# Kernel optimization log

Hardware: AMD Instinct MI355X
Metric: run time of the kernel (lower is better)

## Reference

```python
import jax, jax.numpy as jnp
import numpy as np

B, S, C, H, F = 4, 2048, 256, 8, 512  # scenes, pillars/scene, embed, heads, ffn hidden
D = C // H


def setup_inputs() -> dict:
    key = jax.random.key(0)
    ks = jax.random.split(key, 6)
    n = lambda k, sh: jax.random.normal(k, sh, jnp.float32) * 0.02
    # batch index sorted, equal-size contiguous segments per scene
    bidx = (jnp.arange(B * S, dtype=jnp.int32) // S)[:, None]
    coords = jnp.concatenate([bidx, jnp.zeros((B * S, 3), jnp.int32)], axis=1)
    return dict(
        pillar_features=jax.random.normal(ks[0], (B * S, C), jnp.float32),
        voxel_coords=coords,
        w_qkv=n(ks[1], (3 * C, C)), b_qkv=jnp.zeros((3 * C,), jnp.float32),
        w_out=n(ks[2], (C, C)), b_out=jnp.zeros((C,), jnp.float32),
        ln1_g=jnp.ones((C,), jnp.float32), ln1_b=jnp.zeros((C,), jnp.float32),
        w1=n(ks[3], (F, C)), b1=jnp.zeros((F,), jnp.float32),
        w2=n(ks[4], (C, F)), b2=jnp.zeros((C,), jnp.float32),
        ln2_g=jnp.ones((C,), jnp.float32), ln2_b=jnp.zeros((C,), jnp.float32),
    )


def _ln(x, g, b):
    m = x.mean(-1, keepdims=True)
    v = x.var(-1, keepdims=True)  # biased var, matches torch LayerNorm
    return (x - m) / jnp.sqrt(v + 1e-5) * g + b


def reference(pillar_features, voxel_coords, w_qkv, b_qkv, w_out, b_out,
              ln1_g, ln1_b, w1, b1, w2, b2, ln2_g, ln2_b):
    # coords[:,0] is sorted with equal-size contiguous segments, so the
    # per-batch mask-gather in the original is exactly a reshape here.
    x = pillar_features.reshape(B, S, C)
    qkv = x @ w_qkv.T + b_qkv                      # [B,S,3C]
    q, k, v = jnp.split(qkv, 3, axis=-1)
    rs = lambda t: t.reshape(B, S, H, D).transpose(0, 2, 1, 3)  # [B,H,S,D]
    q, k, v = rs(q), rs(k), rs(v)
    scores = jnp.einsum('bhqd,bhkd->bhqk', q, k) / jnp.sqrt(jnp.float32(D))
    att = jax.nn.softmax(scores, axis=-1)
    o = jnp.einsum('bhqk,bhkd->bhqd', att, v).transpose(0, 2, 1, 3).reshape(B, S, C)
    o = o @ w_out.T + b_out
    x = _ln(x + o, ln1_g, ln1_b)
    f = jax.nn.gelu(x @ w1.T + b1, approximate=False) @ w2.T + b2
    x = _ln(x + f, ln2_g, ln2_b)
    return x.reshape(B * S, C)
```

## Files before the change

### kernel.cpp

```cpp
#include <hip/hip_runtime.h>
#include <math.h>

#define MROWS 8192
#define BATCH 4
#define SEQ   2048
#define CDIM  256
#define HEADS 8
#define DHEAD 32
#define FDIM  512
#define QKVN  768

typedef __attribute__((ext_vector_type(8))) short bf16x8;
typedef __attribute__((ext_vector_type(4))) float f32x4;

__device__ __forceinline__ unsigned pk_bf16(float a, float b) {
  unsigned r;
  asm("v_cvt_pk_bf16_f32 %0, %1, %2" : "=v"(r) : "v"(a), "v"(b));
  return r;
}
__device__ __forceinline__ float bf2f(short s) {
  unsigned u = ((unsigned)(unsigned short)s) << 16;
  return __builtin_bit_cast(float, u);
}
__device__ __forceinline__ float bflo(unsigned w) {
  return __builtin_bit_cast(float, w << 16);
}
__device__ __forceinline__ float bfhi(unsigned w) {
  return __builtin_bit_cast(float, w & 0xffff0000u);
}
__device__ __forceinline__ short f2bf(float f) {
  unsigned u = __builtin_bit_cast(unsigned, f);
  u = (u + 0x7FFFu + ((u >> 16) & 1u)) >> 16;
  return (short)u;
}
__device__ __forceinline__ float fexp2(float x) {
#if __has_builtin(__builtin_amdgcn_exp2f)
  return __builtin_amdgcn_exp2f(x);
#else
  return exp2f(x);
#endif
}
__device__ __forceinline__ void gl16(const void* g, void* l) {
  __builtin_amdgcn_global_load_lds(
      (const __attribute__((address_space(1))) void*)g,
      (__attribute__((address_space(3))) void*)l, 16, 0, 0);
}
__device__ __forceinline__ float gelu_tanh(float v) {
  const float u = v * (0.7978845608f + 0.0356774081f * v * v);
  const float t = fexp2(u * 2.885390082f);
  return v * t / (t + 1.0f);
}

__global__ __launch_bounds__(256) void cast_all_k(
    const float* __restrict__ pillar, short* __restrict__ pb,
    const float* __restrict__ wq, short* __restrict__ wqb,
    const float* __restrict__ wo, short* __restrict__ wob,
    const float* __restrict__ w1, short* __restrict__ w1b,
    const float* __restrict__ w2, short* __restrict__ w2b)
{
  const int i = blockIdx.x * 256 + threadIdx.x;
  const float* s; short* d; int off;
  if (i < 524288)      { s = pillar; d = pb;  off = i; }
  else if (i < 573440) { s = wq;     d = wqb; off = i - 524288; }
  else if (i < 589824) { s = wo;     d = wob; off = i - 573440; }
  else if (i < 622592) { s = w1;     d = w1b; off = i - 589824; }
  else                 { s = w2;     d = w2b; off = i - 622592; }
  float4 v = reinterpret_cast<const float4*>(s)[off];
  uint2 o = { pk_bf16(v.x, v.y), pk_bf16(v.z, v.w) };
  *reinterpret_cast<uint2*>(d + off*4) = o;
}

template<int K, bool BF16OUT, bool GELU, bool VOUT>
__global__ __launch_bounds__(256) void gemm64_k(
    const short* __restrict__ A, const short* __restrict__ W,
    const float* __restrict__ bias, void* __restrict__ out,
    short* __restrict__ vt, int NS)
{
  __shared__ short AS[2][4096];
  __shared__ short WS[2][4096];
  const int tid = threadIdx.x;
  const int l   = tid & 63;
  const int w   = tid >> 6;
  const int m0 = blockIdx.x * 64;
  const int n0 = blockIdx.y * 64;
  const int wr = (w >> 1) * 32;
  const int wc = (w & 1) * 32;
  const int lr = l & 15;
  const int lg = l >> 4;

  f32x4 acc[2][2];
#pragma unroll
  for (int i = 0; i < 2; ++i)
#pragma unroll
    for (int j = 0; j < 2; ++j) acc[i][j] = (f32x4){0.f,0.f,0.f,0.f};

  auto stage = [&](int buf, int k0) {
#pragma unroll
    for (int i = 0; i < 2; ++i) {
      const int c = i*256 + tid;
      const int r = c >> 3;
      const int s = (c & 7) ^ (r & 7);
      gl16(A + (size_t)(m0 + r)*K + k0 + s*8, &AS[buf][c*8]);
      gl16(W + (size_t)(n0 + r)*K + k0 + s*8, &WS[buf][c*8]);
    }
  };

  stage(0, 0);
  const int NST = K / 64;
  for (int t = 0; t < NST; ++t) {
    const int buf = t & 1;
    __syncthreads();
    if (t + 1 < NST) stage(buf ^ 1, (t+1)*64);
#pragma unroll
    for (int ks = 0; ks < 2; ++ks) {
      const int sl = ((ks*4 + lg) ^ (lr & 7)) << 3;
      bf16x8 a[2], b[2];
#pragma unroll
      for (int mi = 0; mi < 2; ++mi)
        a[mi] = *reinterpret_cast<const bf16x8*>(&AS[buf][(wr + mi*16 + lr)*64 + sl]);
#pragma unroll
      for (int nj = 0; nj < 2; ++nj)
        b[nj] = *reinterpret_cast<const bf16x8*>(&WS[buf][(wc + nj*16 + lr)*64 + sl]);
#pragma unroll
      for (int mi = 0; mi < 2; ++mi)
#pragma unroll
        for (int nj = 0; nj < 2; ++nj)
          acc[mi][nj] = __builtin_amdgcn_mfma_f32_16x16x32_bf16(b[nj], a[mi], acc[mi][nj], 0, 0, 0);
    }
  }

#pragma unroll
  for (int mi = 0; mi < 2; ++mi) {
    const size_t m = m0 + wr + mi*16 + lr;
#pragma unroll
    for (int nj = 0; nj < 2; ++nj) {
      const int nf = n0 + wc + nj*16 + lg*4;
      float4 bs = *reinterpret_cast<const float4*>(&bias[nf]);
      f32x4 v = acc[mi][nj];
      float v0 = v[0]+bs.x, v1 = v[1]+bs.y, v2 = v[2]+bs.z, v3 = v[3]+bs.w;
      if (GELU) { v0 = gelu_tanh(v0); v1 = gelu_tanh(v1); v2 = gelu_tanh(v2); v3 = gelu_tanh(v3); }
      if (VOUT && n0 >= 512) {
        const int nl = nf - 512;
        const int hh = nl >> 5, dvb = nl & 31;
        const int bb = (int)(m >> 11), ss = (int)(m & 2047);
        short* vp = vt + ((size_t)((bb*8 + hh)*32 + dvb))*2048 + ss;
        vp[0] = f2bf(v0); vp[2048] = f2bf(v1); vp[4096] = f2bf(v2); vp[6144] = f2bf(v3);
      } else if (BF16OUT) {
        uint2 p = { pk_bf16(v0, v1), pk_bf16(v2, v3) };
        *reinterpret_cast<uint2*>((short*)out + m*NS + nf) = p;
      } else {
        float4 p = { v0, v1, v2, v3 };
        *reinterpret_cast<float4*>((float*)out + m*NS + nf) = p;
      }
    }
  }
}

__global__ __launch_bounds__(512, 8) void attn_mfma_k(
    const short* __restrict__ qk, const short* __restrict__ vtg,
    short* __restrict__ attno)
{
  __shared__ short KS[2][2][2048];
  __shared__ short VS[2][2][2048];

  const int tid  = threadIdx.x;
  const int lane = tid & 63;
  const int wv   = tid >> 6;
  const int st   = wv >> 2;
  const int qw   = wv & 3;
  const int bh   = blockIdx.y;
  const int b    = bh >> 3, h = bh & 7;
  const int q0   = blockIdx.x * 64 + qw * 16;

  const int lr = lane & 15;
  const int lg = lane >> 4;

  bf16x8 qf;
  {
    bf16x8 qraw = *reinterpret_cast<const bf16x8*>(
        qk + (size_t)(b*SEQ + q0 + lr)*512 + h*DHEAD + lg*8);
    const float c = 0.25508134f;
#pragma unroll
    for (int j = 0; j < 8; ++j) qf[j] = f2bf(bf2f(qraw[j]) * c);
  }
  bf16x8 ones;
#pragma unroll
  for (int j = 0; j < 8; ++j) ones[j] = (short)0x3F80;

  f32x4 o0 = {0.f,0.f,0.f,0.f}, o1 = {0.f,0.f,0.f,0.f};
  f32x4 lacc = {0.f,0.f,0.f,0.f};

  const int t256 = tid & 255;
  const short* kSrc;
  {
    const int r = t256 >> 2, s = t256 & 3;
    const int rr = r & 31;
    const int key = ((rr >> 2) & 3)*8 + ((rr >> 4) & 1)*4 + (rr & 3) + (r & 32);
    const int slog = s ^ ((r >> 1) & 3);
    kSrc = qk + (size_t)(b*SEQ + st*1024 + key)*512 + 256 + h*DHEAD + slog*8;
  }
  const short* vSrc;
  {
    const int r = t256 >> 3, s = t256 & 7;
    const int slog = s ^ (r & 7);
    vSrc = vtg + ((size_t)(bh*32 + r))*2048 + st*1024 + slog*8;
  }

  gl16(kSrc, &KS[st][0][t256*8]);
  gl16(vSrc, &VS[st][0][t256*8]);
  kSrc += 64*512; vSrc += 64;

  const int kxor = (lr >> 1) & 3;
  const int vxor = lr & 7;

  for (int t = 0; t < 16; ++t) {
    const int buf = t & 1;
    __syncthreads();
    if (t + 1 < 16) {
      gl16(kSrc, &KS[st][buf^1][t256*8]);
      gl16(vSrc, &VS[st][buf^1][t256*8]);
      kSrc += 64*512; vSrc += 64;
    }

#pragma unroll
    for (int half = 0; half < 2; ++half) {
      const int krow = (half*32 + lr)*32 + ((lg ^ kxor) << 3);
      bf16x8 kf0 = *reinterpret_cast<const bf16x8*>(&KS[st][buf][krow]);
      bf16x8 kf1 = *reinterpret_cast<const bf16x8*>(&KS[st][buf][krow + 512]);
      f32x4 z = {0.f,0.f,0.f,0.f};
      f32x4 s0 = __builtin_amdgcn_mfma_f32_16x16x32_bf16(kf0, qf, z, 0, 0, 0);
      f32x4 s1 = __builtin_amdgcn_mfma_f32_16x16x32_bf16(kf1, qf, z, 0, 0, 0);

      const int vcol = (((half*4 + lg) ^ vxor) << 3);
      bf16x8 vf0 = *reinterpret_cast<const bf16x8*>(&VS[st][buf][lr*64 + vcol]);
      bf16x8 vf1 = *reinterpret_cast<const bf16x8*>(&VS[st][buf][(lr+16)*64 + vcol]);

      float p0 = fexp2(s0[0]), p1 = fexp2(s0[1]), p2 = fexp2(s0[2]), p3 = fexp2(s0[3]);
      float p4 = fexp2(s1[0]), p5 = fexp2(s1[1]), p6 = fexp2(s1[2]), p7 = fexp2(s1[3]);
      union { bf16x8 v; unsigned w[4]; } pfu;
      pfu.w[0] = pk_bf16(p0, p1); pfu.w[1] = pk_bf16(p2, p3);
      pfu.w[2] = pk_bf16(p4, p5); pfu.w[3] = pk_bf16(p6, p7);

      o0   = __builtin_amdgcn_mfma_f32_16x16x32_bf16(vf0, pfu.v, o0, 0, 0, 0);
      o1   = __builtin_amdgcn_mfma_f32_16x16x32_bf16(vf1, pfu.v, o1, 0, 0, 0);
      lacc = __builtin_amdgcn_mfma_f32_16x16x32_bf16(ones, pfu.v, lacc, 0, 0, 0);
    }
  }

  __syncthreads();
  float* mg = (float*)&KS[0][0][0];
  const int mi = (qw*64 + lane)*10;
  if (st == 1) {
    mg[mi+0]=o0[0]; mg[mi+1]=o0[1]; mg[mi+2]=o0[2]; mg[mi+3]=o0[3];
    mg[mi+4]=o1[0]; mg[mi+5]=o1[1]; mg[mi+6]=o1[2]; mg[mi+7]=o1[3];
    mg[mi+8]=lacc[0];
  }
  __syncthreads();
  if (st == 0) {
    const float inv = 1.f / (lacc[0] + mg[mi+8]);
    float a0 = (o0[0]+mg[mi+0])*inv, a1 = (o0[1]+mg[mi+1])*inv;
    float a2 = (o0[2]+mg[mi+2])*inv, a3 = (o0[3]+mg[mi+3])*inv;
    float b0 = (o1[0]+mg[mi+4])*inv, b1 = (o1[1]+mg[mi+5])*inv;
    float b2 = (o1[2]+mg[mi+6])*inv, b3 = (o1[3]+mg[mi+7])*inv;
    short* op = attno + (size_t)(b*SEQ + q0 + lr)*CDIM + h*DHEAD;
    uint2 r0 = { pk_bf16(a0, a1), pk_bf16(a2, a3) };
    uint2 r1 = { pk_bf16(b0, b1), pk_bf16(b2, b3) };
    *reinterpret_cast<uint2*>(op + lg*4)      = r0;
    *reinterpret_cast<uint2*>(op + 16 + lg*4) = r1;
  }
}

template<bool F32OUT>
__global__ __launch_bounds__(256) void resid_lnb_k(
    const short* __restrict__ x, const short* __restrict__ y,
    const float* __restrict__ g, const float* __restrict__ bta,
    float* __restrict__ outf, short* __restrict__ outb)
{
  const int row  = blockIdx.x * 4 + (threadIdx.x >> 6);
  const int lane = threadIdx.x & 63;
  const int c0   = lane * 4;
  const size_t base = (size_t)row * CDIM + c0;
  uint2 xv = *reinterpret_cast<const uint2*>(&x[base]);
  uint2 yv = *reinterpret_cast<const uint2*>(&y[base]);
  float4 v = { bflo(xv.x)+bflo(yv.x), bfhi(xv.x)+bfhi(yv.x),
               bflo(xv.y)+bflo(yv.y), bfhi(xv.y)+bfhi(yv.y) };
  float s  = v.x + v.y + v.z + v.w;
  float sq = v.x*v.x + v.y*v.y + v.z*v.z + v.w*v.w;
#pragma unroll
  for (int off = 1; off < 64; off <<= 1) {
    s  += __shfl_xor(s,  off);
    sq += __shfl_xor(sq, off);
  }
  const float mean = s * (1.f/CDIM);
  const float var  = sq * (1.f/CDIM) - mean*mean;
  const float rstd = rsqrtf(var + 1e-5f);
  float4 gv = *reinterpret_cast<const float4*>(&g[c0]);
  float4 bv = *reinterpret_cast<const float4*>(&bta[c0]);
  float4 r = { (v.x-mean)*rstd*gv.x + bv.x, (v.y-mean)*rstd*gv.y + bv.y,
               (v.z-mean)*rstd*gv.z + bv.z, (v.w-mean)*rstd*gv.w + bv.w };
  if (F32OUT) {
    *reinterpret_cast<float4*>(&outf[base]) = r;
  } else {
    uint2 p = { pk_bf16(r.x, r.y), pk_bf16(r.z, r.w) };
    *reinterpret_cast<uint2*>(outb + base) = p;
  }
}

extern "C" void kernel_launch(void* const* d_in, const int* in_sizes, int n_in,
                              void* d_out, int out_size, void* d_ws, size_t ws_size,
                              hipStream_t stream)
{
  const float* pillar = (const float*)d_in[0];
  const float* w_qkv  = (const float*)d_in[2];
  const float* b_qkv  = (const float*)d_in[3];
  const float* w_out  = (const float*)d_in[4];
  const float* b_out  = (const float*)d_in[5];
  const float* ln1_g  = (const float*)d_in[6];
  const float* ln1_b  = (const float*)d_in[7];
  const float* w1     = (const float*)d_in[8];
  const float* b1     = (const float*)d_in[9];
  const float* w2     = (const float*)d_in[10];
  const float* b2     = (const float*)d_in[11];
  const float* ln2_g  = (const float*)d_in[12];
  const float* ln2_b  = (const float*)d_in[13];
  float* out = (float*)d_out;
  short* sb  = (short*)d_ws;

  short* pb    = sb;
  short* wqb   = sb + 2097152;
  short* wob   = sb + 2293760;
  short* w1b   = sb + 2359296;
  short* w2b   = sb + 2490368;
  short* qk    = sb + 2621440;
  short* vtg   = sb + 6815744;
  short* attnb = sb + 8912896;
  short* x1b   = sb + 2621440;
  short* po    = sb + 6815744;
  short* yhidb = sb + 4718592;
  short* f2b   = sb + 8912896;

  cast_all_k<<<2560, 256, 0, stream>>>(pillar, pb, w_qkv, wqb, w_out, wob,
                                       w1, w1b, w2, w2b);

  gemm64_k<CDIM, true, false, true><<<dim3(MROWS/64, QKVN/64), 256, 0, stream>>>(
      pb, wqb, b_qkv, qk, vtg, 512);

  attn_mfma_k<<<dim3(SEQ/64, BATCH*HEADS), 512, 0, stream>>>(qk, vtg, attnb);

  gemm64_k<CDIM, true, false, false><<<dim3(MROWS/64, CDIM/64), 256, 0, stream>>>(
      attnb, wob, b_out, po, nullptr, CDIM);

  resid_lnb_k<false><<<dim3(MROWS/4), 256, 0, stream>>>(pb, po, ln1_g, ln1_b, nullptr, x1b);

  gemm64_k<CDIM, true, true, false><<<dim3(MROWS/64, FDIM/64), 256, 0, stream>>>(
      x1b, w1b, b1, yhidb, nullptr, FDIM);

  gemm64_k<FDIM, true, false, false><<<dim3(MROWS/64, CDIM/64), 256, 0, stream>>>(
      yhidb, w2b, b2, f2b, nullptr, CDIM);

  resid_lnb_k<true><<<dim3(MROWS/4), 256, 0, stream>>>(x1b, f2b, ln2_g, ln2_b, out, nullptr);
}
```

Before: 82.69 us.

## Fuse output and FFN2 GEMMs with residual-add LayerNorm epilogue

Replaces the separate out-projection GEMM + residual LayerNorm and the FFN2 GEMM + residual LayerNorm with one kernel each. A new 32-row by 256-column GEMM tile covers the full channel width, so each block can compute row mean and variance across its waves through shared memory and apply LayerNorm in the epilogue. This removes two kernel launches and the bf16 round-trips of the intermediate GEMM outputs. In exchange it uses only 256 blocks, each staging the full weight slice per K-step with heavy shared memory use, which may lower occupancy and parallelism.

```diff
diff --git a/kernel.cpp b/kernel.cpp
--- a/kernel.cpp
+++ b/kernel.cpp
@@ -270,39 +270,103 @@
   }
 }
 
-template<bool F32OUT>
-__global__ __launch_bounds__(256) void resid_lnb_k(
-    const short* __restrict__ x, const short* __restrict__ y,
+template<int K, bool F32OUT>
+__global__ __launch_bounds__(512, 4) void gemmln_k(
+    const short* __restrict__ A, const short* __restrict__ W,
+    const float* __restrict__ bias, const short* __restrict__ resid,
     const float* __restrict__ g, const float* __restrict__ bta,
     float* __restrict__ outf, short* __restrict__ outb)
 {
-  const int row  = blockIdx.x * 4 + (threadIdx.x >> 6);
-  const int lane = threadIdx.x & 63;
-  const int c0   = lane * 4;
-  const size_t base = (size_t)row * CDIM + c0;
-  uint2 xv = *reinterpret_cast<const uint2*>(&x[base]);
-  uint2 yv = *reinterpret_cast<const uint2*>(&y[base]);
-  float4 v = { bflo(xv.x)+bflo(yv.x), bfhi(xv.x)+bfhi(yv.x),
-               bflo(xv.y)+bflo(yv.y), bfhi(xv.y)+bfhi(yv.y) };
-  float s  = v.x + v.y + v.z + v.w;
-  float sq = v.x*v.x + v.y*v.y + v.z*v.z + v.w*v.w;
-#pragma unroll
-  for (int off = 1; off < 64; off <<= 1) {
-    s  += __shfl_xor(s,  off);
-    sq += __shfl_xor(sq, off);
-  }
-  const float mean = s * (1.f/CDIM);
-  const float var  = sq * (1.f/CDIM) - mean*mean;
+  __shared__ short AS[2][2048];
+  __shared__ short WS[2][16384];
+  __shared__ float P[32][4][2];
+  const int tid = threadIdx.x;
+  const int l   = tid & 63;
+  const int wv  = tid >> 6;
+  const int wm  = wv >> 2;
+  const int wn  = wv & 3;
+  const int m0  = blockIdx.x * 32;
+  const int lr  = l & 15;
+  const int lg  = l >> 4;
+
+  f32x4 acc[4];
+#pragma unroll
+  for (int j = 0; j < 4; ++j) acc[j] = (f32x4){0.f,0.f,0.f,0.f};
+
+  auto stage = [&](int buf, int k0) {
+    if (tid < 256) {
+      const int r = tid >> 3;
+      const int s = (tid & 7) ^ (r & 7);
+      gl16(A + (size_t)(m0 + r)*K + k0 + s*8, &AS[buf][tid*8]);
+    }
+#pragma unroll
+    for (int i = 0; i < 4; ++i) {
+      const int c = i*512 + tid;
+      const int r = c >> 3;
+      const int s = (c & 7) ^ (r & 7);
+      gl16(W + (size_t)r*K + k0 + s*8, &WS[buf][c*8]);
+    }
+  };
+
+  stage(0, 0);
+  const int NST = K / 64;
+  for (int t = 0; t < NST; ++t) {
+    const int buf = t & 1;
+    __syncthreads();
+    if (t + 1 < NST) stage(buf ^ 1, (t+1)*64);
+#pragma unroll
+    for (int ks = 0; ks < 2; ++ks) {
+      const int sl = ((ks*4 + lg) ^ (lr & 7)) << 3;
+      bf16x8 a = *reinterpret_cast<const bf16x8*>(&AS[buf][(wm*16 + lr)*64 + sl]);
+#pragma unroll
+      for (int nj = 0; nj < 4; ++nj) {
+        bf16x8 b = *reinterpret_cast<const bf16x8*>(&WS[buf][(wn*64 + nj*16 + lr)*64 + sl]);
+        acc[nj] = __builtin_amdgcn_mfma_f32_16x16x32_bf16(b, a, acc[nj], 0, 0, 0);
+      }
+    }
+  }
+
+  const int m = m0 + wm*16 + lr;
+  float vals[16];
+  float s = 0.f, sq = 0.f;
+#pragma unroll
+  for (int nj = 0; nj < 4; ++nj) {
+    const int col = wn*64 + nj*16 + lg*4;
+    float4 bs = *reinterpret_cast<const float4*>(&bias[col]);
+    uint2 rv = *reinterpret_cast<const uint2*>(&resid[(size_t)m*CDIM + col]);
+    float v0 = acc[nj][0] + bs.x + bflo(rv.x);
+    float v1 = acc[nj][1] + bs.y + bfhi(rv.x);
+    float v2 = acc[nj][2] + bs.z + bflo(rv.y);
+    float v3 = acc[nj][3] + bs.w + bfhi(rv.y);
+    vals[nj*4+0]=v0; vals[nj*4+1]=v1; vals[nj*4+2]=v2; vals[nj*4+3]=v3;
+    s += (v0+v1)+(v2+v3);
+    sq += (v0*v0+v1*v1)+(v2*v2+v3*v3);
+  }
+  s  += __shfl_xor(s, 16);  s  += __shfl_xor(s, 32);
+  sq += __shfl_xor(sq, 16); sq += __shfl_xor(sq, 32);
+  if (lg == 0) { P[wm*16 + lr][wn][0] = s; P[wm*16 + lr][wn][1] = sq; }
+  __syncthreads();
+  const float S  = P[wm*16+lr][0][0] + P[wm*16+lr][1][0] + P[wm*16+lr][2][0] + P[wm*16+lr][3][0];
+  const float SQ = P[wm*16+lr][0][1] + P[wm*16+lr][1][1] + P[wm*16+lr][2][1] + P[wm*16+lr][3][1];
+  const float mean = S * (1.f/CDIM);
+  const float var  = SQ * (1.f/CDIM) - mean*mean;
   const float rstd = rsqrtf(var + 1e-5f);
-  float4 gv = *reinterpret_cast<const float4*>(&g[c0]);
-  float4 bv = *reinterpret_cast<const float4*>(&bta[c0]);
-  float4 r = { (v.x-mean)*rstd*gv.x + bv.x, (v.y-mean)*rstd*gv.y + bv.y,
-               (v.z-mean)*rstd*gv.z + bv.z, (v.w-mean)*rstd*gv.w + bv.w };
-  if (F32OUT) {
-    *reinterpret_cast<float4*>(&outf[base]) = r;
-  } else {
-    uint2 p = { pk_bf16(r.x, r.y), pk_bf16(r.z, r.w) };
-    *reinterpret_cast<uint2*>(outb + base) = p;
+#pragma unroll
+  for (int nj = 0; nj < 4; ++nj) {
+    const int col = wn*64 + nj*16 + lg*4;
+    float4 gv = *reinterpret_cast<const float4*>(&g[col]);
+    float4 bv = *reinterpret_cast<const float4*>(&bta[col]);
+    float r0 = (vals[nj*4+0]-mean)*rstd*gv.x + bv.x;
+    float r1 = (vals[nj*4+1]-mean)*rstd*gv.y + bv.y;
+    float r2 = (vals[nj*4+2]-mean)*rstd*gv.z + bv.z;
+    float r3 = (vals[nj*4+3]-mean)*rstd*gv.w + bv.w;
+    if (F32OUT) {
+      float4 p = { r0, r1, r2, r3 };
+      *reinterpret_cast<float4*>(&outf[(size_t)m*CDIM + col]) = p;
+    } else {
+      uint2 p = { pk_bf16(r0, r1), pk_bf16(r2, r3) };
+      *reinterpret_cast<uint2*>(outb + (size_t)m*CDIM + col) = p;
+    }
   }
 }
 
@@ -335,9 +399,7 @@
   short* vtg   = sb + 6815744;
   short* attnb = sb + 8912896;
   short* x1b   = sb + 2621440;
-  short* po    = sb + 6815744;
   short* yhidb = sb + 4718592;
-  short* f2b   = sb + 8912896;
 
   cast_all_k<<<2560, 256, 0, stream>>>(pillar, pb, w_qkv, wqb, w_out, wob,
                                        w1, w1b, w2, w2b);
@@ -347,16 +409,12 @@
 
   attn_mfma_k<<<dim3(SEQ/64, BATCH*HEADS), 512, 0, stream>>>(qk, vtg, attnb);
 
-  gemm64_k<CDIM, true, false, false><<<dim3(MROWS/64, CDIM/64), 256, 0, stream>>>(
-      attnb, wob, b_out, po, nullptr, CDIM);
-
-  resid_lnb_k<false><<<dim3(MROWS/4), 256, 0, stream>>>(pb, po, ln1_g, ln1_b, nullptr, x1b);
+  gemmln_k<CDIM, false><<<dim3(MROWS/32), 512, 0, stream>>>(
+      attnb, wob, b_out, pb, ln1_g, ln1_b, nullptr, x1b);
 
   gemm64_k<CDIM, true, true, false><<<dim3(MROWS/64, FDIM/64), 256, 0, stream>>>(
       x1b, w1b, b1, yhidb, nullptr, FDIM);
 
-  gemm64_k<FDIM, true, false, false><<<dim3(MROWS/64, CDIM/64), 256, 0, stream>>>(
-      yhidb, w2b, b2, f2b, nullptr, CDIM);
-
-  resid_lnb_k<true><<<dim3(MROWS/4), 256, 0, stream>>>(x1b, f2b, ln2_g, ln2_b, out, nullptr);
-}
+  gemmln_k<FDIM, true><<<dim3(MROWS/32), 512, 0, stream>>>(
+      yhidb, w2b, b2, x1b, ln2_g, ln2_b, out, nullptr);
+}
```

New measurement: 83.08 us. About the same (+0.5%).
